# Optimization experiments

Measured on AMD Instinct MI355X. Metric: run time of the kernel, lower is better.

The kernel has to match this reference:

```python
import jax, jax.numpy as jnp
import numpy as np

# physics constants (match PDELoss defaults)
RHO, CP, VZ, KT = 0.3, 1200.0, 0.5, 0.06
# Arrhenius-style soot source constants (representative RadiationPINN.soot_source_terms)
A_NUC, E_NUC = 1.0e4, 2.0e4
A_GROW, E_GROW = 5.0e3, 1.2e4
A_OX, E_OX = 1.0e5, 1.6e4

N, IN_DIM, H, OUT, N_FUELS, EMB = 262144, 12, 128, 7, 4, 8


def mlp(X, emb_rows, W1, b1, W2, b2, W3, b3, Wo, bo):
    # X: (N,4) coords; emb_rows: (N,8) fuel embedding -> T (N,1), fv (N,1), Y (N,5)
    h = jnp.concatenate([X, emb_rows], axis=-1)
    h = jnp.tanh(h @ W1 + b1)
    h = jnp.tanh(h @ W2 + b2)
    h = jnp.tanh(h @ W3 + b3)
    o = h @ Wo + bo
    T = 300.0 + 2000.0 * jax.nn.sigmoid(o[:, 0:1])
    fv = jax.nn.softplus(o[:, 1:2]) * 1e-6
    Y = jax.nn.softmax(o[:, 2:7], axis=-1)
    return T, fv, Y


def soot_sources(T, Y_prec, Y_O2, fv):
    nuc = A_NUC * Y_prec * jnp.exp(-E_NUC / T)
    grow = A_GROW * Y_prec * fv * jnp.exp(-E_GROW / T)
    ox = A_OX * Y_O2 * fv * jnp.sqrt(T) * jnp.exp(-E_OX / T)
    return nuc, grow, ox


def pde_loss(inputs, fuel_ids, W1, b1, W2, b2, W3, b3, Wo, bo, emb):
    emb_rows = emb[fuel_ids]  # (N, EMB), constant w.r.t. inputs
    params = (W1, b1, W2, b2, W3, b3, Wo, bo)

    def T_of(X):
        return mlp(X, emb_rows, *params)[0]

    def fv_of(X):
        return mlp(X, emb_rows, *params)[1]

    n = inputs.shape[0]
    Ez = jnp.zeros_like(inputs).at[:, 1].set(1.0)  # direction d/dz
    Er = jnp.zeros_like(inputs).at[:, 2].set(1.0)  # direction d/dr

    # forward-mode (Taylor) derivatives: nested jvp gives 1st and 2nd order in one pass
    dT_dz_fn = lambda X: jax.jvp(T_of, (X,), (Ez,))[1]
    dT_dz, d2T_dz2 = jax.jvp(dT_dz_fn, (inputs,), (Ez,))
    dT_dr_fn = lambda X: jax.jvp(T_of, (X,), (Er,))[1]
    dT_dr, d2T_dr2 = jax.jvp(dT_dr_fn, (inputs,), (Er,))
    _, dfv_dz = jax.jvp(fv_of, (inputs,), (Ez,))

    T, fv, Y = mlp(inputs, emb_rows, *params)
    Y_prec, Y_O2 = Y[:, 3:4], Y[:, 4:5]

    r = inputs[:, 2:3]
    r_safe = jnp.maximum(r, 1e-6)
    laplacian_r = d2T_dr2 + dT_dr / r_safe
    energy_res = RHO * CP * VZ * dT_dz - KT * laplacian_r - KT * d2T_dz2

    nuc, grow, ox = soot_sources(T, Y_prec, Y_O2, fv)
    soot_res = VZ * dfv_dz - nuc - grow + ox

    loss_energy = jnp.mean(energy_res ** 2)
    loss_soot = jnp.mean(soot_res ** 2)
    return jnp.stack([loss_energy, loss_soot, loss_energy + loss_soot])


def setup_inputs() -> dict:
    key = jax.random.key(0)
    ks = jax.random.split(key, 12)
    inputs = jax.random.uniform(ks[0], (N, 4), dtype=jnp.float32)
    fuel_ids = jax.random.randint(ks[1], (N,), 0, N_FUELS)
    s1, sh, so = 1.0 / np.sqrt(IN_DIM), 1.0 / np.sqrt(H), 1.0 / np.sqrt(H)
    return {
        "inputs": inputs,
        "fuel_ids": fuel_ids,
        "W1": jax.random.normal(ks[2], (IN_DIM, H), jnp.float32) * s1,
        "b1": jnp.zeros((H,), jnp.float32),
        "W2": jax.random.normal(ks[3], (H, H), jnp.float32) * sh,
        "b2": jnp.zeros((H,), jnp.float32),
        "W3": jax.random.normal(ks[4], (H, H), jnp.float32) * sh,
        "b3": jnp.zeros((H,), jnp.float32),
        "Wo": jax.random.normal(ks[5], (H, OUT), jnp.float32) * so,
        "bo": jnp.zeros((OUT,), jnp.float32),
        "emb": jax.random.normal(ks[6], (N_FUELS, EMB), jnp.float32) * 0.1,
    }


def reference(inputs, fuel_ids, W1, b1, W2, b2, W3, b3, Wo, bo, emb):
    return pde_loss(inputs, fuel_ids, W1, b1, W2, b2, W3, b3, Wo, bo, emb)
```

## Files before the change

kernel.cpp:

```cpp
#include <hip/hip_runtime.h>
#include <math.h>

#define NPTS 262144
#define PTS  16
#define NBLK (NPTS / PTS)

typedef _Float16 f16;
typedef f16    f16x4 __attribute__((ext_vector_type(4)));
typedef f16    f16x8 __attribute__((ext_vector_type(8)));
typedef __fp16 h16x2 __attribute__((ext_vector_type(2)));
typedef __fp16 h16x4 __attribute__((ext_vector_type(4)));
typedef float  f32x4 __attribute__((ext_vector_type(4)));


__device__ __forceinline__ h16x2 pk(float a, float b) {
    return __builtin_amdgcn_cvt_pkrtz(a, b);
}
__device__ __forceinline__ f16x4 mrg(h16x2 lo, h16x2 hi) {
    h16x4 v = __builtin_shufflevector(lo, hi, 0, 1, 2, 3);
    return __builtin_bit_cast(f16x4, v);
}

__device__ __forceinline__ float fast_tanh(float z) {
    float e = __expf(2.f * z);
    float r = __builtin_amdgcn_rcpf(e + 1.f);
    return __builtin_fmaf(-2.f, r, 1.f);
}

__global__ void prep_weights(const float* __restrict__ W1, const float* __restrict__ W2,
                             const float* __restrict__ W3, const float* __restrict__ Wo,
                             const float* __restrict__ bo,
                             f16* __restrict__ wt1, f16* __restrict__ wt2,
                             f16* __restrict__ wt3, f16* __restrict__ wot,
                             float* __restrict__ bot)
{
    int tid    = blockIdx.x * blockDim.x + threadIdx.x;
    int stride = gridDim.x * blockDim.x;
    for (int i = tid; i < 128 * 32; i += stride) {
        int k = i >> 7, n = i & 127;
        wt1[n * 32 + k] = (f16)((k < 12) ? W1[k * 128 + n] : 0.f);
    }
    for (int i = tid; i < 128 * 128; i += stride) {
        int k = i >> 7, n = i & 127;
        wt2[n * 128 + k] = (f16)W2[i];
        wt3[n * 128 + k] = (f16)W3[i];
    }
    for (int i = tid; i < 16 * 128; i += stride) {
        int k = i >> 4, n = i & 15;
        wot[n * 128 + k] = (f16)((n < 7) ? Wo[k * 7 + n] : 0.f);
    }
    if (tid < 16) bot[tid] = (tid < 7) ? bo[tid] : 0.f;
}

__device__ __forceinline__ void transform_store(
    char* sA, const f32x4 acc[5], int pt, int n0q)
{
    float t[4], s[4];
#pragma unroll
    for (int r = 0; r < 4; ++r) {
        t[r] = fast_tanh(acc[0][r]);
        s[r] = 1.f - t[r] * t[r];
    }
    h16x2 T[2]  = { pk(t[0], t[1]), pk(t[2], t[3]) };
    h16x2 S[2]  = { pk(s[0], s[1]), pk(s[2], s[3]) };
    h16x2 A1[2] = { pk(acc[1][0], acc[1][1]), pk(acc[1][2], acc[1][3]) };
    h16x2 A2[2] = { pk(acc[2][0], acc[2][1]), pk(acc[2][2], acc[2][3]) };
    h16x2 A3[2] = { pk(acc[3][0], acc[3][1]), pk(acc[3][2], acc[3][3]) };
    h16x2 A4[2] = { pk(acc[4][0], acc[4][1]), pk(acc[4][2], acc[4][3]) };
    h16x2 TZ[2], TZZ[2], TR[2], TRR[2];
#pragma unroll
    for (int p = 0; p < 2; ++p) {
        h16x2 n2t = -(T[p] + T[p]);
        TZ[p]  = S[p] * A1[p];
        TR[p]  = S[p] * A3[p];
        TZZ[p] = n2t * (TZ[p] * A1[p]) + S[p] * A2[p];
        TRR[p] = n2t * (TR[p] * A3[p]) + S[p] * A4[p];
    }
    const int key = (pt & 7) << 4;
    char* rb = sA + (pt << 8) + (((n0q * 2)) ^ key);
    *(f16x4*)(rb)         = mrg(T[0], T[1]);
    *(f16x4*)(rb +  4096) = mrg(TZ[0], TZ[1]);
    *(f16x4*)(rb +  8192) = mrg(TZZ[0], TZZ[1]);
    *(f16x4*)(rb + 12288) = mrg(TR[0], TR[1]);
    *(f16x4*)(rb + 16384) = mrg(TRR[0], TRR[1]);
}

__device__ __forceinline__ void transform_store_l1(
    char* sA, const f32x4 acc0, const f32x4 wz, const f32x4 wr,
    int pt, int n0q)
{
    float t[4], s[4];
#pragma unroll
    for (int r = 0; r < 4; ++r) {
        t[r] = fast_tanh(acc0[r]);
        s[r] = 1.f - t[r] * t[r];
    }
    h16x2 T[2]  = { pk(t[0], t[1]), pk(t[2], t[3]) };
    h16x2 S[2]  = { pk(s[0], s[1]), pk(s[2], s[3]) };
    h16x2 A1[2] = { pk(wz[0], wz[1]), pk(wz[2], wz[3]) };
    h16x2 A3[2] = { pk(wr[0], wr[1]), pk(wr[2], wr[3]) };
    h16x2 TZ[2], TZZ[2], TR[2], TRR[2];
#pragma unroll
    for (int p = 0; p < 2; ++p) {
        h16x2 n2t = -(T[p] + T[p]);
        TZ[p]  = S[p] * A1[p];
        TR[p]  = S[p] * A3[p];
        TZZ[p] = n2t * (TZ[p] * A1[p]);
        TRR[p] = n2t * (TR[p] * A3[p]);
    }
    const int key = (pt & 7) << 4;
    char* rb = sA + (pt << 8) + (((n0q * 2)) ^ key);
    *(f16x4*)(rb)         = mrg(T[0], T[1]);
    *(f16x4*)(rb +  4096) = mrg(TZ[0], TZ[1]);
    *(f16x4*)(rb +  8192) = mrg(TZZ[0], TZZ[1]);
    *(f16x4*)(rb + 12288) = mrg(TR[0], TR[1]);
    *(f16x4*)(rb + 16384) = mrg(TRR[0], TRR[1]);
}

__device__ __forceinline__ void layer128(
    char* sA, const f16* __restrict__ Wt, const float* __restrict__ b,
    int q, int m)
{
    const int mkey = (m & 7) << 4;
    const char* rp = sA + (m << 8);
    f16x8 Bv[5][4];
#pragma unroll
    for (int c = 0; c < 5; ++c)
#pragma unroll
        for (int kt = 0; kt < 4; ++kt)
            Bv[c][kt] = *(const f16x8*)(rp + c * 4096 + ((kt * 64 + q * 16) ^ mkey));

    const f32x4 z4 = {0.f, 0.f, 0.f, 0.f};
#pragma unroll
    for (int ct0 = 0; ct0 < 8; ++ct0) {
        const int n0 = ct0 * 16;
        const f16* wp = &Wt[(n0 + m) * 128 + q * 8];
        f16x8 A0 = *(const f16x8*)(wp);
        f16x8 A1 = *(const f16x8*)(wp + 32);
        f16x8 A2 = *(const f16x8*)(wp + 64);
        f16x8 A3 = *(const f16x8*)(wp + 96);
        f32x4 bb = *(const f32x4*)&b[n0 + q * 4];
        f32x4 acc[5];
        acc[0] = __builtin_amdgcn_mfma_f32_16x16x32_f16(A0, Bv[0][0], bb, 0, 0, 0);
#pragma unroll
        for (int c = 1; c < 5; ++c) acc[c] = __builtin_amdgcn_mfma_f32_16x16x32_f16(A0, Bv[c][0], z4, 0, 0, 0);
#pragma unroll
        for (int c = 0; c < 5; ++c) acc[c] = __builtin_amdgcn_mfma_f32_16x16x32_f16(A1, Bv[c][1], acc[c], 0, 0, 0);
#pragma unroll
        for (int c = 0; c < 5; ++c) acc[c] = __builtin_amdgcn_mfma_f32_16x16x32_f16(A2, Bv[c][2], acc[c], 0, 0, 0);
#pragma unroll
        for (int c = 0; c < 5; ++c) acc[c] = __builtin_amdgcn_mfma_f32_16x16x32_f16(A3, Bv[c][3], acc[c], 0, 0, 0);

        transform_store(sA, acc, m, n0 + q * 4);
    }
}

__global__ __launch_bounds__(64, 2) void pde_main(
    const float* __restrict__ X,
    const int*   __restrict__ fid,
    const float* __restrict__ emb,
    const float* __restrict__ W1,
    const float* __restrict__ b1, const float* __restrict__ b2,
    const float* __restrict__ b3,
    const f16* __restrict__ Wt1, const f16* __restrict__ Wt2,
    const f16* __restrict__ Wt3, const f16* __restrict__ Wot,
    const float* __restrict__ bot,
    float* __restrict__ partials)
{
    __shared__ f32x4 smem4[1280];
    char* sA = (char*)smem4;

    const int lane = threadIdx.x;
    const int q    = lane >> 4;
    const int m    = lane & 15;
    const int p0   = blockIdx.x * PTS;

    float rcoord = 0.f;
    if (lane < PTS) {
        const int p = lane;
        f32x4 xr = *(const f32x4*)&X[(p0 + p) * 4];
        rcoord = xr.z;
        const float* er = &emb[fid[p0 + p] * 8];
        f32x4 e0 = *(const f32x4*)er;
        f32x4 e1 = *(const f32x4*)(er + 4);
        const f16x4 zz = {(f16)0.f, (f16)0.f, (f16)0.f, (f16)0.f};
        const int key = (p & 7) << 4;
        char* rb = sA + (p << 8);
        *(f16x4*)(rb + (0  ^ key)) = mrg(pk(xr.x, xr.y), pk(xr.z, xr.w));
        *(f16x4*)(rb + (8  ^ key)) = mrg(pk(e0.x, e0.y), pk(e0.z, e0.w));
        *(f16x4*)(rb + (16 ^ key)) = mrg(pk(e1.x, e1.y), pk(e1.z, e1.w));
        *(f16x4*)(rb + (24 ^ key)) = zz;
        *(f16x4*)(rb + (32 ^ key)) = zz;
        *(f16x4*)(rb + (40 ^ key)) = zz;
        *(f16x4*)(rb + (48 ^ key)) = zz;
        *(f16x4*)(rb + (56 ^ key)) = zz;
    }

    {
        const int mkey = (m & 7) << 4;
        f16x8 Bv0 = *(const f16x8*)(sA + (m << 8) + ((q * 16) ^ mkey));
#pragma unroll
        for (int ct0 = 0; ct0 < 8; ++ct0) {
            const int n0 = ct0 * 16;
            f16x8 A0 = *(const f16x8*)&Wt1[(n0 + m) * 32 + q * 8];
            f32x4 bb = *(const f32x4*)&b1[n0 + q * 4];
            f32x4 acc0 = __builtin_amdgcn_mfma_f32_16x16x32_f16(A0, Bv0, bb, 0, 0, 0);
            f32x4 wz = *(const f32x4*)&W1[128 + n0 + q * 4];
            f32x4 wr = *(const f32x4*)&W1[256 + n0 + q * 4];
            transform_store_l1(sA, acc0, wz, wr, m, n0 + q * 4);
        }
    }

    layer128(sA, Wt2, b2, q, m);
    layer128(sA, Wt3, b3, q, m);

    f32x4 acc[5];
    {
        const int mkey = (m & 7) << 4;
        const char* rp = sA + (m << 8);
        f16x8 Bh[5][4];
#pragma unroll
        for (int c = 0; c < 5; ++c)
#pragma unroll
            for (int kt = 0; kt < 4; ++kt)
                Bh[c][kt] = *(const f16x8*)(rp + c * 4096 + ((kt * 64 + q * 16) ^ mkey));
        f32x4 c0i = *(const f32x4*)&bot[q * 4];
        const f16* wp = &Wot[m * 128 + q * 8];
        f16x8 A0 = *(const f16x8*)(wp);
        f16x8 A1 = *(const f16x8*)(wp + 32);
        f16x8 A2 = *(const f16x8*)(wp + 64);
        f16x8 A3 = *(const f16x8*)(wp + 96);
        const f32x4 z4 = {0.f, 0.f, 0.f, 0.f};
        acc[0] = __builtin_amdgcn_mfma_f32_16x16x32_f16(A0, Bh[0][0], c0i, 0, 0, 0);
#pragma unroll
        for (int c = 1; c < 5; ++c) acc[c] = __builtin_amdgcn_mfma_f32_16x16x32_f16(A0, Bh[c][0], z4, 0, 0, 0);
#pragma unroll
        for (int c = 0; c < 5; ++c) acc[c] = __builtin_amdgcn_mfma_f32_16x16x32_f16(A1, Bh[c][1], acc[c], 0, 0, 0);
#pragma unroll
        for (int c = 0; c < 5; ++c) acc[c] = __builtin_amdgcn_mfma_f32_16x16x32_f16(A2, Bh[c][2], acc[c], 0, 0, 0);
#pragma unroll
        for (int c = 0; c < 5; ++c) acc[c] = __builtin_amdgcn_mfma_f32_16x16x32_f16(A3, Bh[c][3], acc[c], 0, 0, 0);
    }
    const int src = (lane & 15) + 16;
    float o4 = __shfl(acc[0][0], src, 64);
    float o5 = __shfl(acc[0][1], src, 64);
    float o6 = __shfl(acc[0][2], src, 64);

    if (lane < PTS) {
        float o0   = acc[0][0], o1  = acc[0][1];
        float o0z  = acc[1][0], o1z = acc[1][1];
        float o0zz = acc[2][0];
        float o0r  = acc[3][0];
        float o0rr = acc[4][0];

        float sg  = __fdividef(1.f, 1.f + __expf(-o0));
        float T   = 300.f + 2000.f * sg;
        float sp  = sg * (1.f - sg);
        float spp = sp * (1.f - 2.f * sg);
        float Tz  = 2000.f * sp * o0z;
        float Tzz = 2000.f * (spp * o0z * o0z + sp * o0zz);
        float Tr  = 2000.f * sp * o0r;
        float Trr = 2000.f * (spp * o0r * o0r + sp * o0rr);

        float rs  = fmaxf(rcoord, 1e-6f);
        float lap = Trr + __fdividef(Tr, rs);
        float eres = 180.f * Tz - 0.06f * lap - 0.06f * Tzz;

        float fv  = ((o1 > 20.f) ? o1 : __logf(1.f + __expf(o1))) * 1e-6f;
        float s1  = __fdividef(1.f, 1.f + __expf(-o1));
        float fvz = s1 * o1z * 1e-6f;

        float y0 = acc[0][2], y1 = acc[0][3], y2 = o4, y3 = o5, y4 = o6;
        float mx = fmaxf(fmaxf(fmaxf(y0, y1), fmaxf(y2, y3)), y4);
        float e0 = __expf(y0 - mx), e1 = __expf(y1 - mx), e2 = __expf(y2 - mx);
        float e3 = __expf(y3 - mx), e4 = __expf(y4 - mx);
        float inv = __fdividef(1.f, e0 + e1 + e2 + e3 + e4);
        float Yp = e3 * inv;
        float Yo = e4 * inv;

        float rT  = __fdividef(1.f, T);
        float nuc  = 1e4f * Yp * __expf(-20000.f * rT);
        float grow = 5e3f * Yp * fv * __expf(-12000.f * rT);
        float ox   = 1e5f * Yo * fv * sqrtf(T) * __expf(-16000.f * rT);
        float sres = 0.5f * fvz - nuc - grow + ox;

        float ve = eres * eres;
        float vs = sres * sres;
#pragma unroll
        for (int o = 8; o > 0; o >>= 1) {
            ve += __shfl_xor(ve, o, 64);
            vs += __shfl_xor(vs, o, 64);
        }
        if (lane == 0) {
            float2 w; w.x = ve; w.y = vs;
            *(float2*)&partials[2 * blockIdx.x] = w;
        }
    }
}

__global__ __launch_bounds__(1024) void pde_finalize(
    const float* __restrict__ partials, float* __restrict__ out)
{
    __shared__ double rE[1024];
    __shared__ double rS[1024];
    const int tid = threadIdx.x;
    const float2* p2 = (const float2*)partials;
    double se = 0.0, ss = 0.0;
    for (int i = tid; i < NBLK; i += 1024) {
        float2 v = p2[i];
        se += (double)v.x;
        ss += (double)v.y;
    }
    rE[tid] = se; rS[tid] = ss;
    __syncthreads();
    for (int s = 512; s > 0; s >>= 1) {
        if (tid < s) { rE[tid] += rE[tid + s]; rS[tid] += rS[tid + s]; }
        __syncthreads();
    }
    if (tid == 0) {
        const double invN = 1.0 / (double)NPTS;
        float le = (float)(rE[0] * invN);
        float ls = (float)(rS[0] * invN);
        out[0] = le;
        out[1] = ls;
        out[2] = le + ls;
    }
}

extern "C" void kernel_launch(void* const* d_in, const int* in_sizes, int n_in,
                              void* d_out, int out_size, void* d_ws, size_t ws_size,
                              hipStream_t stream)
{
    const float* X   = (const float*)d_in[0];
    const int*   fid = (const int*)  d_in[1];
    const float* W1  = (const float*)d_in[2];
    const float* b1  = (const float*)d_in[3];
    const float* W2  = (const float*)d_in[4];
    const float* b2  = (const float*)d_in[5];
    const float* W3  = (const float*)d_in[6];
    const float* b3  = (const float*)d_in[7];
    const float* Wo  = (const float*)d_in[8];
    const float* bo  = (const float*)d_in[9];
    const float* emb = (const float*)d_in[10];

    f16*   wt1      = (f16*)d_ws;
    f16*   wt2      = wt1 + 128 * 32;
    f16*   wt3      = wt2 + 128 * 128;
    f16*   wot      = wt3 + 128 * 128;
    float* bot      = (float*)(wot + 16 * 128);
    float* partials = bot + 16;
    float* out      = (float*)d_out;

    prep_weights<<<128, 256, 0, stream>>>(W1, W2, W3, Wo, bo, wt1, wt2, wt3, wot, bot);
    pde_main<<<NBLK, 64, 0, stream>>>(X, fid, emb, W1, b1, b2, b3,
                                      wt1, wt2, wt3, wot, bot, partials);
    pde_finalize<<<1, 1024, 0, stream>>>(partials, out);
}
```

Measured before the change: 236.4 us.

## Make main kernel persistent over point groups with next-group input prefetch

Launches 2048 blocks instead of 16384, and each block loops over 8 groups of 16 points with a grid stride. While the current group's coordinates and embeddings are staged into shared memory, the next group's global loads are issued so their latency overlaps the MLP compute. This cuts block launch overhead and hides the input load latency. In exchange there are fewer waves in flight (2048 single-wave blocks across the CUs), possible register pressure from the loop-carried prefetch, and no barrier between the end of one group's shared-memory reads and the next group's writes.

Result: slower. 521.1 us (+120.5%).

```diff
diff --git a/kernel.cpp b/kernel.cpp
--- a/kernel.cpp
+++ b/kernel.cpp
@@ -1,9 +1,11 @@
 #include <hip/hip_runtime.h>
 #include <math.h>
 
-#define NPTS 262144
-#define PTS  16
-#define NBLK (NPTS / PTS)
+#define NPTS   262144
+#define PTS    16
+#define NBLK   (NPTS / PTS)
+#define NBLK_P 2048
+#define GRP    (NBLK / NBLK_P)
 
 typedef _Float16 f16;
 typedef f16    f16x4 __attribute__((ext_vector_type(4)));
@@ -173,127 +175,144 @@
     const int lane = threadIdx.x;
     const int q    = lane >> 4;
     const int m    = lane & 15;
-    const int p0   = blockIdx.x * PTS;
-
-    float rcoord = 0.f;
-    if (lane < PTS) {
-        const int p = lane;
-        f32x4 xr = *(const f32x4*)&X[(p0 + p) * 4];
-        rcoord = xr.z;
-        const float* er = &emb[fid[p0 + p] * 8];
-        f32x4 e0 = *(const f32x4*)er;
-        f32x4 e1 = *(const f32x4*)(er + 4);
-        const f16x4 zz = {(f16)0.f, (f16)0.f, (f16)0.f, (f16)0.f};
-        const int key = (p & 7) << 4;
-        char* rb = sA + (p << 8);
-        *(f16x4*)(rb + (0  ^ key)) = mrg(pk(xr.x, xr.y), pk(xr.z, xr.w));
-        *(f16x4*)(rb + (8  ^ key)) = mrg(pk(e0.x, e0.y), pk(e0.z, e0.w));
-        *(f16x4*)(rb + (16 ^ key)) = mrg(pk(e1.x, e1.y), pk(e1.z, e1.w));
-        *(f16x4*)(rb + (24 ^ key)) = zz;
-        *(f16x4*)(rb + (32 ^ key)) = zz;
-        *(f16x4*)(rb + (40 ^ key)) = zz;
-        *(f16x4*)(rb + (48 ^ key)) = zz;
-        *(f16x4*)(rb + (56 ^ key)) = zz;
-    }
-
-    {
-        const int mkey = (m & 7) << 4;
-        f16x8 Bv0 = *(const f16x8*)(sA + (m << 8) + ((q * 16) ^ mkey));
-#pragma unroll
-        for (int ct0 = 0; ct0 < 8; ++ct0) {
-            const int n0 = ct0 * 16;
-            f16x8 A0 = *(const f16x8*)&Wt1[(n0 + m) * 32 + q * 8];
-            f32x4 bb = *(const f32x4*)&b1[n0 + q * 4];
-            f32x4 acc0 = __builtin_amdgcn_mfma_f32_16x16x32_f16(A0, Bv0, bb, 0, 0, 0);
-            f32x4 wz = *(const f32x4*)&W1[128 + n0 + q * 4];
-            f32x4 wr = *(const f32x4*)&W1[256 + n0 + q * 4];
-            transform_store_l1(sA, acc0, wz, wr, m, n0 + q * 4);
-        }
-    }
-
-    layer128(sA, Wt2, b2, q, m);
-    layer128(sA, Wt3, b3, q, m);
-
-    f32x4 acc[5];
-    {
-        const int mkey = (m & 7) << 4;
-        const char* rp = sA + (m << 8);
-        f16x8 Bh[5][4];
-#pragma unroll
-        for (int c = 0; c < 5; ++c)
-#pragma unroll
-            for (int kt = 0; kt < 4; ++kt)
-                Bh[c][kt] = *(const f16x8*)(rp + c * 4096 + ((kt * 64 + q * 16) ^ mkey));
-        f32x4 c0i = *(const f32x4*)&bot[q * 4];
-        const f16* wp = &Wot[m * 128 + q * 8];
-        f16x8 A0 = *(const f16x8*)(wp);
-        f16x8 A1 = *(const f16x8*)(wp + 32);
-        f16x8 A2 = *(const f16x8*)(wp + 64);
-        f16x8 A3 = *(const f16x8*)(wp + 96);
-        const f32x4 z4 = {0.f, 0.f, 0.f, 0.f};
-        acc[0] = __builtin_amdgcn_mfma_f32_16x16x32_f16(A0, Bh[0][0], c0i, 0, 0, 0);
-#pragma unroll
-        for (int c = 1; c < 5; ++c) acc[c] = __builtin_amdgcn_mfma_f32_16x16x32_f16(A0, Bh[c][0], z4, 0, 0, 0);
-#pragma unroll
-        for (int c = 0; c < 5; ++c) acc[c] = __builtin_amdgcn_mfma_f32_16x16x32_f16(A1, Bh[c][1], acc[c], 0, 0, 0);
-#pragma unroll
-        for (int c = 0; c < 5; ++c) acc[c] = __builtin_amdgcn_mfma_f32_16x16x32_f16(A2, Bh[c][2], acc[c], 0, 0, 0);
-#pragma unroll
-        for (int c = 0; c < 5; ++c) acc[c] = __builtin_amdgcn_mfma_f32_16x16x32_f16(A3, Bh[c][3], acc[c], 0, 0, 0);
-    }
-    const int src = (lane & 15) + 16;
-    float o4 = __shfl(acc[0][0], src, 64);
-    float o5 = __shfl(acc[0][1], src, 64);
-    float o6 = __shfl(acc[0][2], src, 64);
-
-    if (lane < PTS) {
-        float o0   = acc[0][0], o1  = acc[0][1];
-        float o0z  = acc[1][0], o1z = acc[1][1];
-        float o0zz = acc[2][0];
-        float o0r  = acc[3][0];
-        float o0rr = acc[4][0];
-
-        float sg  = __fdividef(1.f, 1.f + __expf(-o0));
-        float T   = 300.f + 2000.f * sg;
-        float sp  = sg * (1.f - sg);
-        float spp = sp * (1.f - 2.f * sg);
-        float Tz  = 2000.f * sp * o0z;
-        float Tzz = 2000.f * (spp * o0z * o0z + sp * o0zz);
-        float Tr  = 2000.f * sp * o0r;
-        float Trr = 2000.f * (spp * o0r * o0r + sp * o0rr);
-
-        float rs  = fmaxf(rcoord, 1e-6f);
-        float lap = Trr + __fdividef(Tr, rs);
-        float eres = 180.f * Tz - 0.06f * lap - 0.06f * Tzz;
-
-        float fv  = ((o1 > 20.f) ? o1 : __logf(1.f + __expf(o1))) * 1e-6f;
-        float s1  = __fdividef(1.f, 1.f + __expf(-o1));
-        float fvz = s1 * o1z * 1e-6f;
-
-        float y0 = acc[0][2], y1 = acc[0][3], y2 = o4, y3 = o5, y4 = o6;
-        float mx = fmaxf(fmaxf(fmaxf(y0, y1), fmaxf(y2, y3)), y4);
-        float e0 = __expf(y0 - mx), e1 = __expf(y1 - mx), e2 = __expf(y2 - mx);
-        float e3 = __expf(y3 - mx), e4 = __expf(y4 - mx);
-        float inv = __fdividef(1.f, e0 + e1 + e2 + e3 + e4);
-        float Yp = e3 * inv;
-        float Yo = e4 * inv;
-
-        float rT  = __fdividef(1.f, T);
-        float nuc  = 1e4f * Yp * __expf(-20000.f * rT);
-        float grow = 5e3f * Yp * fv * __expf(-12000.f * rT);
-        float ox   = 1e5f * Yo * fv * sqrtf(T) * __expf(-16000.f * rT);
-        float sres = 0.5f * fvz - nuc - grow + ox;
-
-        float ve = eres * eres;
-        float vs = sres * sres;
-#pragma unroll
-        for (int o = 8; o > 0; o >>= 1) {
-            ve += __shfl_xor(ve, o, 64);
-            vs += __shfl_xor(vs, o, 64);
-        }
-        if (lane == 0) {
-            float2 w; w.x = ve; w.y = vs;
-            *(float2*)&partials[2 * blockIdx.x] = w;
+    const bool ld  = (lane < PTS);
+
+    f32x4 xr = {0.f, 0.f, 0.f, 0.f};
+    f32x4 e0 = xr, e1 = xr;
+    if (ld) {
+        const int p = blockIdx.x * PTS + lane;
+        xr = *(const f32x4*)&X[p * 4];
+        const float* er = &emb[fid[p] * 8];
+        e0 = *(const f32x4*)er;
+        e1 = *(const f32x4*)(er + 4);
+    }
+
+#pragma unroll 1
+    for (int g = 0; g < GRP; ++g) {
+        const int gid = blockIdx.x + g * NBLK_P;
+
+        float rcoord = xr.z;
+        if (ld) {
+            const int p = m;
+            const f16x4 zz = {(f16)0.f, (f16)0.f, (f16)0.f, (f16)0.f};
+            const int key = (p & 7) << 4;
+            char* rb = sA + (p << 8);
+            *(f16x4*)(rb + (0  ^ key)) = mrg(pk(xr.x, xr.y), pk(xr.z, xr.w));
+            *(f16x4*)(rb + (8  ^ key)) = mrg(pk(e0.x, e0.y), pk(e0.z, e0.w));
+            *(f16x4*)(rb + (16 ^ key)) = mrg(pk(e1.x, e1.y), pk(e1.z, e1.w));
+            *(f16x4*)(rb + (24 ^ key)) = zz;
+            *(f16x4*)(rb + (32 ^ key)) = zz;
+            *(f16x4*)(rb + (40 ^ key)) = zz;
+            *(f16x4*)(rb + (48 ^ key)) = zz;
+            *(f16x4*)(rb + (56 ^ key)) = zz;
+        }
+        if (ld && g + 1 < GRP) {
+            const int pn = (blockIdx.x + (g + 1) * NBLK_P) * PTS + lane;
+            xr = *(const f32x4*)&X[pn * 4];
+            const float* er = &emb[fid[pn] * 8];
+            e0 = *(const f32x4*)er;
+            e1 = *(const f32x4*)(er + 4);
+        }
+
+        {
+            const int mkey = (m & 7) << 4;
+            f16x8 Bv0 = *(const f16x8*)(sA + (m << 8) + ((q * 16) ^ mkey));
+#pragma unroll
+            for (int ct0 = 0; ct0 < 8; ++ct0) {
+                const int n0 = ct0 * 16;
+                f16x8 A0 = *(const f16x8*)&Wt1[(n0 + m) * 32 + q * 8];
+                f32x4 bb = *(const f32x4*)&b1[n0 + q * 4];
+                f32x4 acc0 = __builtin_amdgcn_mfma_f32_16x16x32_f16(A0, Bv0, bb, 0, 0, 0);
+                f32x4 wz = *(const f32x4*)&W1[128 + n0 + q * 4];
+                f32x4 wr = *(const f32x4*)&W1[256 + n0 + q * 4];
+                transform_store_l1(sA, acc0, wz, wr, m, n0 + q * 4);
+            }
+        }
+
+        layer128(sA, Wt2, b2, q, m);
+        layer128(sA, Wt3, b3, q, m);
+
+        f32x4 acc[5];
+        {
+            const int mkey = (m & 7) << 4;
+            const char* rp = sA + (m << 8);
+            f16x8 Bh[5][4];
+#pragma unroll
+            for (int c = 0; c < 5; ++c)
+#pragma unroll
+                for (int kt = 0; kt < 4; ++kt)
+                    Bh[c][kt] = *(const f16x8*)(rp + c * 4096 + ((kt * 64 + q * 16) ^ mkey));
+            f32x4 c0i = *(const f32x4*)&bot[q * 4];
+            const f16* wp = &Wot[m * 128 + q * 8];
+            f16x8 A0 = *(const f16x8*)(wp);
+            f16x8 A1 = *(const f16x8*)(wp + 32);
+            f16x8 A2 = *(const f16x8*)(wp + 64);
+            f16x8 A3 = *(const f16x8*)(wp + 96);
+            const f32x4 z4 = {0.f, 0.f, 0.f, 0.f};
+            acc[0] = __builtin_amdgcn_mfma_f32_16x16x32_f16(A0, Bh[0][0], c0i, 0, 0, 0);
+#pragma unroll
+            for (int c = 1; c < 5; ++c) acc[c] = __builtin_amdgcn_mfma_f32_16x16x32_f16(A0, Bh[c][0], z4, 0, 0, 0);
+#pragma unroll
+            for (int c = 0; c < 5; ++c) acc[c] = __builtin_amdgcn_mfma_f32_16x16x32_f16(A1, Bh[c][1], acc[c], 0, 0, 0);
+#pragma unroll
+            for (int c = 0; c < 5; ++c) acc[c] = __builtin_amdgcn_mfma_f32_16x16x32_f16(A2, Bh[c][2], acc[c], 0, 0, 0);
+#pragma unroll
+            for (int c = 0; c < 5; ++c) acc[c] = __builtin_amdgcn_mfma_f32_16x16x32_f16(A3, Bh[c][3], acc[c], 0, 0, 0);
+        }
+        const int src = (lane & 15) + 16;
+        float o4 = __shfl(acc[0][0], src, 64);
+        float o5 = __shfl(acc[0][1], src, 64);
+        float o6 = __shfl(acc[0][2], src, 64);
+
+        if (ld) {
+            float o0   = acc[0][0], o1  = acc[0][1];
+            float o0z  = acc[1][0], o1z = acc[1][1];
+            float o0zz = acc[2][0];
+            float o0r  = acc[3][0];
+            float o0rr = acc[4][0];
+
+            float sg  = __fdividef(1.f, 1.f + __expf(-o0));
+            float T   = 300.f + 2000.f * sg;
+            float sp  = sg * (1.f - sg);
+            float spp = sp * (1.f - 2.f * sg);
+            float Tz  = 2000.f * sp * o0z;
+            float Tzz = 2000.f * (spp * o0z * o0z + sp * o0zz);
+            float Tr  = 2000.f * sp * o0r;
+            float Trr = 2000.f * (spp * o0r * o0r + sp * o0rr);
+
+            float rs  = fmaxf(rcoord, 1e-6f);
+            float lap = Trr + __fdividef(Tr, rs);
+            float eres = 180.f * Tz - 0.06f * lap - 0.06f * Tzz;
+
+            float fv  = ((o1 > 20.f) ? o1 : __logf(1.f + __expf(o1))) * 1e-6f;
+            float s1  = __fdividef(1.f, 1.f + __expf(-o1));
+            float fvz = s1 * o1z * 1e-6f;
+
+            float y0 = acc[0][2], y1 = acc[0][3], y2 = o4, y3 = o5, y4 = o6;
+            float mx = fmaxf(fmaxf(fmaxf(y0, y1), fmaxf(y2, y3)), y4);
+            float e0s = __expf(y0 - mx), e1s = __expf(y1 - mx), e2s = __expf(y2 - mx);
+            float e3s = __expf(y3 - mx), e4s = __expf(y4 - mx);
+            float inv = __fdividef(1.f, e0s + e1s + e2s + e3s + e4s);
+            float Yp = e3s * inv;
+            float Yo = e4s * inv;
+
+            float rT  = __fdividef(1.f, T);
+            float nuc  = 1e4f * Yp * __expf(-20000.f * rT);
+            float grow = 5e3f * Yp * fv * __expf(-12000.f * rT);
+            float ox   = 1e5f * Yo * fv * sqrtf(T) * __expf(-16000.f * rT);
+            float sres = 0.5f * fvz - nuc - grow + ox;
+
+            float ve = eres * eres;
+            float vs = sres * sres;
+#pragma unroll
+            for (int o = 8; o > 0; o >>= 1) {
+                ve += __shfl_xor(ve, o, 64);
+                vs += __shfl_xor(vs, o, 64);
+            }
+            if (lane == 0) {
+                float2 w; w.x = ve; w.y = vs;
+                *(float2*)&partials[2 * gid] = w;
+            }
         }
     }
 }
@@ -352,7 +371,7 @@
     float* out      = (float*)d_out;
 
     prep_weights<<<128, 256, 0, stream>>>(W1, W2, W3, Wo, bo, wt1, wt2, wt3, wot, bot);
-    pde_main<<<NBLK, 64, 0, stream>>>(X, fid, emb, W1, b1, b2, b3,
-                                      wt1, wt2, wt3, wot, bot, partials);
+    pde_main<<<NBLK_P, 64, 0, stream>>>(X, fid, emb, W1, b1, b2, b3,
+                                        wt1, wt2, wt3, wot, bot, partials);
     pde_finalize<<<1, 1024, 0, stream>>>(partials, out);
 }
```

## Process two 16-point tiles per wavefront to reuse weight fragments

Applied to the files above, without the earlier changes.

Each 64-thread block now handles 32 points as two independent 16-point tiles held in separate LDS buffers. Every loaded weight fragment feeds two MFMA chains, halving global/L2 weight traffic per point and giving the matrix unit two independent accumulator streams to interleave. The cost is double the LDS per block (40 KB), many more live VGPRs for the B operands and accumulators, and launch_bounds lowered to one wave per SIMD, which may cut occupancy and latency hiding.

Result: slower. 244.7 us (+3.5%).

```diff
diff --git a/kernel.cpp b/kernel.cpp
--- a/kernel.cpp
+++ b/kernel.cpp
@@ -1,9 +1,11 @@
 #include <hip/hip_runtime.h>
 #include <math.h>
 
-#define NPTS 262144
-#define PTS  16
-#define NBLK (NPTS / PTS)
+#define NPTS  262144
+#define PTS   16
+#define PTS2  32
+#define NBLK  (NPTS / PTS)
+#define NBLK2 (NPTS / PTS2)
 
 typedef _Float16 f16;
 typedef f16    f16x4 __attribute__((ext_vector_type(4)));
@@ -117,18 +119,22 @@
     *(f16x4*)(rb + 16384) = mrg(TRR[0], TRR[1]);
 }
 
-__device__ __forceinline__ void layer128(
-    char* sA, const f16* __restrict__ Wt, const float* __restrict__ b,
+__device__ __forceinline__ void layer128_dual(
+    char* sA, char* sB, const f16* __restrict__ Wt, const float* __restrict__ b,
     int q, int m)
 {
     const int mkey = (m & 7) << 4;
-    const char* rp = sA + (m << 8);
-    f16x8 Bv[5][4];
+    const char* rpA = sA + (m << 8);
+    const char* rpB = sB + (m << 8);
+    f16x8 BvA[5][4], BvB[5][4];
 #pragma unroll
     for (int c = 0; c < 5; ++c)
 #pragma unroll
-        for (int kt = 0; kt < 4; ++kt)
-            Bv[c][kt] = *(const f16x8*)(rp + c * 4096 + ((kt * 64 + q * 16) ^ mkey));
+        for (int kt = 0; kt < 4; ++kt) {
+            const int off = (kt * 64 + q * 16) ^ mkey;
+            BvA[c][kt] = *(const f16x8*)(rpA + c * 4096 + off);
+            BvB[c][kt] = *(const f16x8*)(rpB + c * 4096 + off);
+        }
 
     const f32x4 z4 = {0.f, 0.f, 0.f, 0.f};
 #pragma unroll
@@ -140,22 +146,35 @@
         f16x8 A2 = *(const f16x8*)(wp + 64);
         f16x8 A3 = *(const f16x8*)(wp + 96);
         f32x4 bb = *(const f32x4*)&b[n0 + q * 4];
-        f32x4 acc[5];
-        acc[0] = __builtin_amdgcn_mfma_f32_16x16x32_f16(A0, Bv[0][0], bb, 0, 0, 0);
-#pragma unroll
-        for (int c = 1; c < 5; ++c) acc[c] = __builtin_amdgcn_mfma_f32_16x16x32_f16(A0, Bv[c][0], z4, 0, 0, 0);
-#pragma unroll
-        for (int c = 0; c < 5; ++c) acc[c] = __builtin_amdgcn_mfma_f32_16x16x32_f16(A1, Bv[c][1], acc[c], 0, 0, 0);
-#pragma unroll
-        for (int c = 0; c < 5; ++c) acc[c] = __builtin_amdgcn_mfma_f32_16x16x32_f16(A2, Bv[c][2], acc[c], 0, 0, 0);
-#pragma unroll
-        for (int c = 0; c < 5; ++c) acc[c] = __builtin_amdgcn_mfma_f32_16x16x32_f16(A3, Bv[c][3], acc[c], 0, 0, 0);
-
-        transform_store(sA, acc, m, n0 + q * 4);
-    }
-}
-
-__global__ __launch_bounds__(64, 2) void pde_main(
+        f32x4 aA[5], aB[5];
+        aA[0] = __builtin_amdgcn_mfma_f32_16x16x32_f16(A0, BvA[0][0], bb, 0, 0, 0);
+        aB[0] = __builtin_amdgcn_mfma_f32_16x16x32_f16(A0, BvB[0][0], bb, 0, 0, 0);
+#pragma unroll
+        for (int c = 1; c < 5; ++c) {
+            aA[c] = __builtin_amdgcn_mfma_f32_16x16x32_f16(A0, BvA[c][0], z4, 0, 0, 0);
+            aB[c] = __builtin_amdgcn_mfma_f32_16x16x32_f16(A0, BvB[c][0], z4, 0, 0, 0);
+        }
+#pragma unroll
+        for (int c = 0; c < 5; ++c) {
+            aA[c] = __builtin_amdgcn_mfma_f32_16x16x32_f16(A1, BvA[c][1], aA[c], 0, 0, 0);
+            aB[c] = __builtin_amdgcn_mfma_f32_16x16x32_f16(A1, BvB[c][1], aB[c], 0, 0, 0);
+        }
+#pragma unroll
+        for (int c = 0; c < 5; ++c) {
+            aA[c] = __builtin_amdgcn_mfma_f32_16x16x32_f16(A2, BvA[c][2], aA[c], 0, 0, 0);
+            aB[c] = __builtin_amdgcn_mfma_f32_16x16x32_f16(A2, BvB[c][2], aB[c], 0, 0, 0);
+        }
+#pragma unroll
+        for (int c = 0; c < 5; ++c) {
+            aA[c] = __builtin_amdgcn_mfma_f32_16x16x32_f16(A3, BvA[c][3], aA[c], 0, 0, 0);
+            aB[c] = __builtin_amdgcn_mfma_f32_16x16x32_f16(A3, BvB[c][3], aB[c], 0, 0, 0);
+        }
+        transform_store(sA, aA, m, n0 + q * 4);
+        transform_store(sB, aB, m, n0 + q * 4);
+    }
+}
+
+__global__ __launch_bounds__(64, 1) void pde_main(
     const float* __restrict__ X,
     const int*   __restrict__ fid,
     const float* __restrict__ emb,
@@ -167,25 +186,27 @@
     const float* __restrict__ bot,
     float* __restrict__ partials)
 {
-    __shared__ f32x4 smem4[1280];
+    __shared__ f32x4 smem4[2560];
     char* sA = (char*)smem4;
+    char* sB = sA + 20480;
 
     const int lane = threadIdx.x;
     const int q    = lane >> 4;
     const int m    = lane & 15;
-    const int p0   = blockIdx.x * PTS;
+    const int p0   = blockIdx.x * PTS2;
 
     float rcoord = 0.f;
-    if (lane < PTS) {
-        const int p = lane;
-        f32x4 xr = *(const f32x4*)&X[(p0 + p) * 4];
+    if (lane < PTS2) {
+        const int p = p0 + lane;
+        f32x4 xr = *(const f32x4*)&X[p * 4];
         rcoord = xr.z;
-        const float* er = &emb[fid[p0 + p] * 8];
+        const float* er = &emb[fid[p] * 8];
         f32x4 e0 = *(const f32x4*)er;
         f32x4 e1 = *(const f32x4*)(er + 4);
         const f16x4 zz = {(f16)0.f, (f16)0.f, (f16)0.f, (f16)0.f};
-        const int key = (p & 7) << 4;
-        char* rb = sA + (p << 8);
+        const int pp  = lane & 15;
+        const int key = (pp & 7) << 4;
+        char* rb = ((lane < PTS) ? sA : sB) + (pp << 8);
         *(f16x4*)(rb + (0  ^ key)) = mrg(pk(xr.x, xr.y), pk(xr.z, xr.w));
         *(f16x4*)(rb + (8  ^ key)) = mrg(pk(e0.x, e0.y), pk(e0.z, e0.w));
         *(f16x4*)(rb + (16 ^ key)) = mrg(pk(e1.x, e1.y), pk(e1.z, e1.w));
@@ -198,32 +219,40 @@
 
     {
         const int mkey = (m & 7) << 4;
-        f16x8 Bv0 = *(const f16x8*)(sA + (m << 8) + ((q * 16) ^ mkey));
+        const int off0 = (q * 16) ^ mkey;
+        f16x8 Bv0A = *(const f16x8*)(sA + (m << 8) + off0);
+        f16x8 Bv0B = *(const f16x8*)(sB + (m << 8) + off0);
 #pragma unroll
         for (int ct0 = 0; ct0 < 8; ++ct0) {
             const int n0 = ct0 * 16;
             f16x8 A0 = *(const f16x8*)&Wt1[(n0 + m) * 32 + q * 8];
             f32x4 bb = *(const f32x4*)&b1[n0 + q * 4];
-            f32x4 acc0 = __builtin_amdgcn_mfma_f32_16x16x32_f16(A0, Bv0, bb, 0, 0, 0);
+            f32x4 aA = __builtin_amdgcn_mfma_f32_16x16x32_f16(A0, Bv0A, bb, 0, 0, 0);
+            f32x4 aB = __builtin_amdgcn_mfma_f32_16x16x32_f16(A0, Bv0B, bb, 0, 0, 0);
             f32x4 wz = *(const f32x4*)&W1[128 + n0 + q * 4];
             f32x4 wr = *(const f32x4*)&W1[256 + n0 + q * 4];
-            transform_store_l1(sA, acc0, wz, wr, m, n0 + q * 4);
-        }
-    }
-
-    layer128(sA, Wt2, b2, q, m);
-    layer128(sA, Wt3, b3, q, m);
-
-    f32x4 acc[5];
+            transform_store_l1(sA, aA, wz, wr, m, n0 + q * 4);
+            transform_store_l1(sB, aB, wz, wr, m, n0 + q * 4);
+        }
+    }
+
+    layer128_dual(sA, sB, Wt2, b2, q, m);
+    layer128_dual(sA, sB, Wt3, b3, q, m);
+
+    f32x4 accA[5], accB[5];
     {
         const int mkey = (m & 7) << 4;
-        const char* rp = sA + (m << 8);
-        f16x8 Bh[5][4];
+        const char* rpA = sA + (m << 8);
+        const char* rpB = sB + (m << 8);
+        f16x8 BhA[5][4], BhB[5][4];
 #pragma unroll
         for (int c = 0; c < 5; ++c)
 #pragma unroll
-            for (int kt = 0; kt < 4; ++kt)
-                Bh[c][kt] = *(const f16x8*)(rp + c * 4096 + ((kt * 64 + q * 16) ^ mkey));
+            for (int kt = 0; kt < 4; ++kt) {
+                const int off = (kt * 64 + q * 16) ^ mkey;
+                BhA[c][kt] = *(const f16x8*)(rpA + c * 4096 + off);
+                BhB[c][kt] = *(const f16x8*)(rpB + c * 4096 + off);
+            }
         f32x4 c0i = *(const f32x4*)&bot[q * 4];
         const f16* wp = &Wot[m * 128 + q * 8];
         f16x8 A0 = *(const f16x8*)(wp);
@@ -231,27 +260,60 @@
         f16x8 A2 = *(const f16x8*)(wp + 64);
         f16x8 A3 = *(const f16x8*)(wp + 96);
         const f32x4 z4 = {0.f, 0.f, 0.f, 0.f};
-        acc[0] = __builtin_amdgcn_mfma_f32_16x16x32_f16(A0, Bh[0][0], c0i, 0, 0, 0);
-#pragma unroll
-        for (int c = 1; c < 5; ++c) acc[c] = __builtin_amdgcn_mfma_f32_16x16x32_f16(A0, Bh[c][0], z4, 0, 0, 0);
-#pragma unroll
-        for (int c = 0; c < 5; ++c) acc[c] = __builtin_amdgcn_mfma_f32_16x16x32_f16(A1, Bh[c][1], acc[c], 0, 0, 0);
-#pragma unroll
-        for (int c = 0; c < 5; ++c) acc[c] = __builtin_amdgcn_mfma_f32_16x16x32_f16(A2, Bh[c][2], acc[c], 0, 0, 0);
-#pragma unroll
-        for (int c = 0; c < 5; ++c) acc[c] = __builtin_amdgcn_mfma_f32_16x16x32_f16(A3, Bh[c][3], acc[c], 0, 0, 0);
-    }
-    const int src = (lane & 15) + 16;
-    float o4 = __shfl(acc[0][0], src, 64);
-    float o5 = __shfl(acc[0][1], src, 64);
-    float o6 = __shfl(acc[0][2], src, 64);
-
-    if (lane < PTS) {
-        float o0   = acc[0][0], o1  = acc[0][1];
-        float o0z  = acc[1][0], o1z = acc[1][1];
-        float o0zz = acc[2][0];
-        float o0r  = acc[3][0];
-        float o0rr = acc[4][0];
+        accA[0] = __builtin_amdgcn_mfma_f32_16x16x32_f16(A0, BhA[0][0], c0i, 0, 0, 0);
+        accB[0] = __builtin_amdgcn_mfma_f32_16x16x32_f16(A0, BhB[0][0], c0i, 0, 0, 0);
+#pragma unroll
+        for (int c = 1; c < 5; ++c) {
+            accA[c] = __builtin_amdgcn_mfma_f32_16x16x32_f16(A0, BhA[c][0], z4, 0, 0, 0);
+            accB[c] = __builtin_amdgcn_mfma_f32_16x16x32_f16(A0, BhB[c][0], z4, 0, 0, 0);
+        }
+#pragma unroll
+        for (int c = 0; c < 5; ++c) {
+            accA[c] = __builtin_amdgcn_mfma_f32_16x16x32_f16(A1, BhA[c][1], accA[c], 0, 0, 0);
+            accB[c] = __builtin_amdgcn_mfma_f32_16x16x32_f16(A1, BhB[c][1], accB[c], 0, 0, 0);
+        }
+#pragma unroll
+        for (int c = 0; c < 5; ++c) {
+            accA[c] = __builtin_amdgcn_mfma_f32_16x16x32_f16(A2, BhA[c][2], accA[c], 0, 0, 0);
+            accB[c] = __builtin_amdgcn_mfma_f32_16x16x32_f16(A2, BhB[c][2], accB[c], 0, 0, 0);
+        }
+#pragma unroll
+        for (int c = 0; c < 5; ++c) {
+            accA[c] = __builtin_amdgcn_mfma_f32_16x16x32_f16(A3, BhA[c][3], accA[c], 0, 0, 0);
+            accB[c] = __builtin_amdgcn_mfma_f32_16x16x32_f16(A3, BhB[c][3], accB[c], 0, 0, 0);
+        }
+    }
+    const int up = (lane & 15) + 16;
+    const int dn = lane & 15;
+
+    float y2A = __shfl(accA[0][0], up, 64);
+    float y3A = __shfl(accA[0][1], up, 64);
+    float y4A = __shfl(accA[0][2], up, 64);
+
+    float bo0   = __shfl(accB[0][0], dn, 64);
+    float bo1   = __shfl(accB[0][1], dn, 64);
+    float by0   = __shfl(accB[0][2], dn, 64);
+    float by1   = __shfl(accB[0][3], dn, 64);
+    float bo0z  = __shfl(accB[1][0], dn, 64);
+    float bo1z  = __shfl(accB[1][1], dn, 64);
+    float bo0zz = __shfl(accB[2][0], dn, 64);
+    float bo0r  = __shfl(accB[3][0], dn, 64);
+    float bo0rr = __shfl(accB[4][0], dn, 64);
+
+    if (lane < PTS2) {
+        const bool isB = (lane >= PTS);
+        float o0   = isB ? bo0   : accA[0][0];
+        float o1   = isB ? bo1   : accA[0][1];
+        float y0   = isB ? by0   : accA[0][2];
+        float y1   = isB ? by1   : accA[0][3];
+        float o0z  = isB ? bo0z  : accA[1][0];
+        float o1z  = isB ? bo1z  : accA[1][1];
+        float o0zz = isB ? bo0zz : accA[2][0];
+        float o0r  = isB ? bo0r  : accA[3][0];
+        float o0rr = isB ? bo0rr : accA[4][0];
+        float y2   = isB ? accB[0][0] : y2A;
+        float y3   = isB ? accB[0][1] : y3A;
+        float y4   = isB ? accB[0][2] : y4A;
 
         float sg  = __fdividef(1.f, 1.f + __expf(-o0));
         float T   = 300.f + 2000.f * sg;
@@ -270,13 +332,12 @@
         float s1  = __fdividef(1.f, 1.f + __expf(-o1));
         float fvz = s1 * o1z * 1e-6f;
 
-        float y0 = acc[0][2], y1 = acc[0][3], y2 = o4, y3 = o5, y4 = o6;
         float mx = fmaxf(fmaxf(fmaxf(y0, y1), fmaxf(y2, y3)), y4);
-        float e0 = __expf(y0 - mx), e1 = __expf(y1 - mx), e2 = __expf(y2 - mx);
-        float e3 = __expf(y3 - mx), e4 = __expf(y4 - mx);
-        float inv = __fdividef(1.f, e0 + e1 + e2 + e3 + e4);
-        float Yp = e3 * inv;
-        float Yo = e4 * inv;
+        float e0s = __expf(y0 - mx), e1s = __expf(y1 - mx), e2s = __expf(y2 - mx);
+        float e3s = __expf(y3 - mx), e4s = __expf(y4 - mx);
+        float inv = __fdividef(1.f, e0s + e1s + e2s + e3s + e4s);
+        float Yp = e3s * inv;
+        float Yo = e4s * inv;
 
         float rT  = __fdividef(1.f, T);
         float nuc  = 1e4f * Yp * __expf(-20000.f * rT);
@@ -291,9 +352,10 @@
             ve += __shfl_xor(ve, o, 64);
             vs += __shfl_xor(vs, o, 64);
         }
-        if (lane == 0) {
+        if ((lane & 15) == 0) {
+            const int gid = blockIdx.x * 2 + (lane >> 4);
             float2 w; w.x = ve; w.y = vs;
-            *(float2*)&partials[2 * blockIdx.x] = w;
+            *(float2*)&partials[2 * gid] = w;
         }
     }
 }
@@ -352,7 +414,7 @@
     float* out      = (float*)d_out;
 
     prep_weights<<<128, 256, 0, stream>>>(W1, W2, W3, Wo, bo, wt1, wt2, wt3, wot, bot);
-    pde_main<<<NBLK, 64, 0, stream>>>(X, fid, emb, W1, b1, b2, b3,
-                                      wt1, wt2, wt3, wot, bot, partials);
+    pde_main<<<NBLK2, 64, 0, stream>>>(X, fid, emb, W1, b1, b2, b3,
+                                       wt1, wt2, wt3, wot, bot, partials);
     pde_finalize<<<1, 1024, 0, stream>>>(partials, out);
 }
```
